# Kernel tuning notes

Measured on AMD Instinct MI355X. Metric: run time of the kernel, lower is better.

The kernel has to match this reference:

```python
import jax, jax.numpy as jnp
import numpy as np

BATCH, SEQ, D_IN, D_HID, D_OUT = 256, 512, 128, 128, 128


def setup_inputs() -> dict:
    key = jax.random.key(0)
    ks = jax.random.split(key, 10)
    def xavier(k, shape):
        std = (2.0 / (shape[0] + shape[1])) ** 0.5
        return jax.random.normal(k, shape, dtype=jnp.float32) * std
    return {
        "x": jax.random.normal(ks[0], (BATCH, SEQ, D_IN), dtype=jnp.float32),
        "x2i": xavier(ks[1], (D_IN, D_HID)),
        "x2f": xavier(ks[2], (D_IN, D_HID)),
        "x2g": xavier(ks[3], (D_IN, D_HID)),
        "x2o": xavier(ks[4], (D_IN, D_HID)),
        "h2i": xavier(ks[5], (D_HID, D_HID)),
        "h2f": xavier(ks[6], (D_HID, D_HID)),
        "h2g": xavier(ks[7], (D_HID, D_HID)),
        "h2o": xavier(ks[8], (D_HID, D_HID)),
        "w_out": xavier(ks[9], (D_HID, D_OUT)),
    }


def reference(x, x2i, x2f, x2g, x2o, h2i, h2f, h2g, h2o, w_out):
    batch = x.shape[0]
    hid = h2i.shape[0]
    # Precompute input projections for all timesteps (same math, hoisted out
    # of the recurrence): [B, S, 4H] -> time-major [S, B, 4H]
    wx = jnp.concatenate([x2i, x2f, x2g, x2o], axis=1)       # [D_IN, 4H]
    wh = jnp.concatenate([h2i, h2f, h2g, h2o], axis=1)       # [H, 4H]
    xg = jnp.einsum("bsi,ik->sbk", x, wx)                    # [S, B, 4H]

    def step(carry, xg_t):
        c, h = carry
        gates = xg_t + h @ wh                                # [B, 4H]
        i = jax.nn.sigmoid(gates[:, 0 * hid:1 * hid])
        f = jax.nn.sigmoid(gates[:, 1 * hid:2 * hid])
        g = jnp.tanh(gates[:, 2 * hid:3 * hid])
        o = jax.nn.sigmoid(gates[:, 3 * hid:4 * hid])
        c = f * c + i * g
        h = o * jnp.tanh(c)
        return (c, h), None

    c0 = jnp.zeros((batch, hid), dtype=x.dtype)
    h0 = jnp.zeros((batch, hid), dtype=x.dtype)
    (c_T, h_T), _ = jax.lax.scan(step, (c0, h0), xg)
    return h_T @ w_out
```

## Files before the change

### kernel.cpp

```cpp
#include <hip/hip_runtime.h>

typedef unsigned int u32;
typedef __fp16 half2_t __attribute__((ext_vector_type(2)));
typedef __fp16 half8_t __attribute__((ext_vector_type(8)));
typedef float  f32x4   __attribute__((ext_vector_type(4)));

#define DIN 128
#define DH  128
#define SEQL 512
#define NBATCH 256
#define NC  512
#define TC  64
#define NCHUNK (SEQL/TC)

#define LDS_HOFF 65536
#define LDS_TOTAL (65536 + 512)

__device__ __forceinline__ u32 pk2(float a, float b) {
  half2_t h = __builtin_amdgcn_cvt_pkrtz(a, b);
  return __builtin_bit_cast(u32, h);
}

__device__ __forceinline__ float dot2(u32 a, u32 b, float c) {
#if defined(__has_builtin) && __has_builtin(__builtin_amdgcn_fdot2)
  return __builtin_amdgcn_fdot2(__builtin_bit_cast(half2_t, a),
                                __builtin_bit_cast(half2_t, b), c, false);
#else
  half2_t ha = __builtin_bit_cast(half2_t, a);
  half2_t hb = __builtin_bit_cast(half2_t, b);
  return c + (float)ha[0]*(float)hb[0] + (float)ha[1]*(float)hb[1];
#endif
}

#if defined(__has_builtin) && __has_builtin(__builtin_amdgcn_update_dpp)
__device__ __forceinline__ float qp_xor1(float v) {
  return __builtin_bit_cast(float,
      __builtin_amdgcn_update_dpp(0, __builtin_bit_cast(int, v), 0xB1, 0xF, 0xF, true));
}
__device__ __forceinline__ float qp_xor2(float v) {
  return __builtin_bit_cast(float,
      __builtin_amdgcn_update_dpp(0, __builtin_bit_cast(int, v), 0x4E, 0xF, 0xF, true));
}
#else
__device__ __forceinline__ float qp_xor1(float v) { return __shfl_xor(v, 1, 64); }
__device__ __forceinline__ float qp_xor2(float v) { return __shfl_xor(v, 2, 64); }
#endif

__device__ __forceinline__ float fexp2(float x) {
#if defined(__has_builtin) && __has_builtin(__builtin_amdgcn_exp2f)
  return __builtin_amdgcn_exp2f(x);
#else
  return __builtin_exp2f(x);
#endif
}

#define DOT16(S, W, H0, H1, H2, H3) \
  S = dot2((W)[0].x, (H0).x, S); S = dot2((W)[0].y, (H0).y, S); \
  S = dot2((W)[0].z, (H0).z, S); S = dot2((W)[0].w, (H0).w, S); \
  S = dot2((W)[1].x, (H1).x, S); S = dot2((W)[1].y, (H1).y, S); \
  S = dot2((W)[1].z, (H1).z, S); S = dot2((W)[1].w, (H1).w, S); \
  S = dot2((W)[2].x, (H2).x, S); S = dot2((W)[2].y, (H2).y, S); \
  S = dot2((W)[2].z, (H2).z, S); S = dot2((W)[2].w, (H2).w, S); \
  S = dot2((W)[3].x, (H3).x, S); S = dot2((W)[3].y, (H3).y, S); \
  S = dot2((W)[3].z, (H3).z, S); S = dot2((W)[3].w, (H3).w, S);

__global__ void pack_w(const float* __restrict__ x2i, const float* __restrict__ x2f,
                       const float* __restrict__ x2g, const float* __restrict__ x2o,
                       const float* __restrict__ h2i, const float* __restrict__ h2f,
                       const float* __restrict__ h2g, const float* __restrict__ h2o,
                       u32* __restrict__ wxT, u32* __restrict__ whT) {
  int idx = blockIdx.x * blockDim.x + threadIdx.x;
  if (idx >= NC * 64) return;
  int j = idx >> 6, kk = idx & 63;
  int g = j >> 7, jjj = j & 127;
  const float* wx = (g == 0) ? x2i : (g == 1) ? x2f : (g == 2) ? x2g : x2o;
  const float* wh = (g == 0) ? h2i : (g == 1) ? h2f : (g == 2) ? h2g : h2o;
  wxT[idx] = pk2(wx[(2*kk)*DH + jjj], wx[(2*kk+1)*DH + jjj]);
  whT[idx] = pk2(wh[(2*kk)*DH + jjj], wh[(2*kk+1)*DH + jjj]);
}

__global__ __launch_bounds__(512, 2) void lstm_fused(
    const float* __restrict__ x, const u32* __restrict__ wxT,
    const u32* __restrict__ whT, const float* __restrict__ w_out,
    float* __restrict__ out) {
  extern __shared__ char lds[];
  char* xgT  = lds;
  u32*  hbuf = (u32*)(lds + LDS_HOFF);

  const int tid = threadIdx.x;
  const int b   = blockIdx.x;
  const int l   = tid & 63, wv = tid >> 6;
  const int kq  = l & 3, jj = l >> 2;
  const int colB = kq * DH + wv * 16 + jj;
  const int j    = wv * 16 + jj;
  const int kg = l >> 4, r15 = l & 15;

  uint4 wq[4][4];
#pragma unroll
  for (int q = 0; q < 4; ++q) {
    const uint4* wp = (const uint4*)(whT + (q * DH + j) * 64 + kq * 16);
#pragma unroll
    for (int mm = 0; mm < 4; ++mm) wq[q][mm] = wp[mm];
  }

  if (tid < 128) hbuf[tid] = 0u;
  float c = 0.f;
  u32 rdoff = LDS_HOFF + kq * 64;
  u32 wroff = LDS_HOFF + 256 + j * 2;
  const bool isG = (kq == 2);
  const float mexp = isG ? -2.885390082f : -1.442695041f;
  const bool k1 = (kq & 1) != 0, k2 = (kq & 2) != 0;

  const float* xb = x + (size_t)b * SEQL * DIN;
  __syncthreads();

  for (int ch = 0; ch < NCHUNK; ++ch) {
#pragma unroll 1
    for (int tt = 0; tt < 4; ++tt) {
      uint4 afr[4];
#pragma unroll
      for (int ko = 0; ko < 4; ++ko) {
        const float4* xp = (const float4*)(xb + (size_t)(ch*TC + tt*16 + r15)*DIN + ko*32 + kg*8);
        float4 v0 = xp[0], v1 = xp[1];
        afr[ko].x = pk2(v0.x, v0.y); afr[ko].y = pk2(v0.z, v0.w);
        afr[ko].z = pk2(v1.x, v1.y); afr[ko].w = pk2(v1.z, v1.w);
      }
#pragma unroll
      for (int nt = 0; nt < 4; ++nt) {
        int n = wv * 64 + nt * 16 + r15;
        f32x4 acc = {0.f, 0.f, 0.f, 0.f};
#pragma unroll
        for (int ko = 0; ko < 4; ++ko) {
          uint4 bf = *(const uint4*)(wxT + n*64 + ko*16 + kg*4);
          acc = __builtin_amdgcn_mfma_f32_16x16x32_f16(
              __builtin_bit_cast(half8_t, afr[ko]),
              __builtin_bit_cast(half8_t, bf), acc, 0, 0, 0);
        }
        int t0 = tt*16 + kg*4;
        u32 off = (u32)(n*128 + ((t0*2) ^ ((n & 7) << 4)));
        uint2 pw; pw.x = pk2(acc[0], acc[1]); pw.y = pk2(acc[2], acc[3]);
        *(uint2*)(xgT + off) = pw;
      }
    }
    __syncthreads();

#pragma unroll 1
    for (int m = 0; m < 8; ++m) {
      uint4 xgv = *(const uint4*)(xgT + colB*128 + ((m*16) ^ ((colB & 7) << 4)));
      half8_t xgh = __builtin_bit_cast(half8_t, xgv);
#pragma unroll
      for (int s8 = 0; s8 < 8; ++s8) {
        uint4 h0 = *(const uint4*)(lds + rdoff);
        uint4 h1 = *(const uint4*)(lds + rdoff + 16);
        uint4 h2 = *(const uint4*)(lds + rdoff + 32);
        uint4 h3 = *(const uint4*)(lds + rdoff + 48);
        float s0 = 0.f, s1 = 0.f, s2 = 0.f, s3 = 0.f;
        DOT16(s0, wq[0], h0, h1, h2, h3)
        DOT16(s1, wq[1], h0, h1, h2, h3)
        DOT16(s2, wq[2], h0, h1, h2, h3)
        DOT16(s3, wq[3], h0, h1, h2, h3)
        s0 += qp_xor1(s0); s0 += qp_xor2(s0);
        s1 += qp_xor1(s1); s1 += qp_xor2(s1);
        s2 += qp_xor1(s2); s2 += qp_xor2(s2);
        s3 += qp_xor1(s3); s3 += qp_xor2(s3);
        float t01 = k1 ? s1 : s0;
        float t23 = k1 ? s3 : s2;
        float tk  = (k2 ? t23 : t01) + (float)xgh[s8];
        float e   = fexp2(tk * mexp);
        float y   = __builtin_amdgcn_rcpf(1.f + e);
        float val = isG ? __builtin_fmaf(2.f, y, -1.f) : y;
        float vb = qp_xor1(val);
        float x0 = k1 ? vb : val;
        float x1 = k1 ? val : vb;
        float y2 = qp_xor2(x0);
        float y3 = qp_xor2(x1);
        float gi = k2 ? y2 : x0;
        float gf = k2 ? y3 : x1;
        float gg = k2 ? x0 : y2;
        float go = k2 ? x1 : y3;
        c = __builtin_fmaf(gf, c, gi * gg);
        float e2 = fexp2(c * -2.885390082f);
        float th = __builtin_fmaf(2.f, __builtin_amdgcn_rcpf(1.f + e2), -1.f);
        float hval = go * th;
        if (kq == 0) *(__fp16*)(lds + wroff) = (__fp16)hval;
        rdoff ^= 256; wroff ^= 256;
        __syncthreads();
      }
    }
  }

  if (tid < DH) {
    int n = tid;
    const u32* hf = (const u32*)(lds + (rdoff & ~(u32)255));
    float acc = 0.f;
#pragma unroll 8
    for (int kk = 0; kk < 64; ++kk) {
      half2_t h2v = __builtin_bit_cast(half2_t, hf[kk]);
      acc = __builtin_fmaf((float)h2v[0], w_out[(2*kk)*DH + n],
            __builtin_fmaf((float)h2v[1], w_out[(2*kk+1)*DH + n], acc));
    }
    out[b * DH + n] = acc;
  }
}

extern "C" void kernel_launch(void* const* d_in, const int* in_sizes, int n_in,
                              void* d_out, int out_size, void* d_ws, size_t ws_size,
                              hipStream_t stream) {
  const float* x    = (const float*)d_in[0];
  const float* x2i  = (const float*)d_in[1];
  const float* x2f  = (const float*)d_in[2];
  const float* x2g  = (const float*)d_in[3];
  const float* x2o  = (const float*)d_in[4];
  const float* h2i  = (const float*)d_in[5];
  const float* h2f  = (const float*)d_in[6];
  const float* h2g  = (const float*)d_in[7];
  const float* h2o  = (const float*)d_in[8];
  const float* wout = (const float*)d_in[9];

  u32* wxT = (u32*)d_ws;
  u32* whT = wxT + NC * 64;

  (void)hipFuncSetAttribute((const void*)lstm_fused,
                            hipFuncAttributeMaxDynamicSharedMemorySize, LDS_TOTAL);

  pack_w<<<64, 512, 0, stream>>>(x2i, x2f, x2g, x2o, h2i, h2f, h2g, h2o, wxT, whT);
  lstm_fused<<<NBATCH, 512, LDS_TOTAL, stream>>>(x, wxT, whT, wout, (float*)d_out);
}
```

Baseline: 319.7 us.

## Compute recurrent gate matvec with MFMA instead of packed dot2 reductions

Replaces the per-step h·Wh product, previously done with fdot2 chains and DPP cross-lane reductions, with 16 MFMA 16x16x32 f16 instructions per wave. Each wave holds its Wh slice as B fragments, and h is broadcast as the A operand. Each lane then computes all four gates directly, so the cross-lane gate shuffles go away. In exchange, each MFMA's output is only one-sixteenth useful, and every lane evaluates five transcendental functions per step instead of two.

```diff
diff --git a/kernel.cpp b/kernel.cpp
--- a/kernel.cpp
+++ b/kernel.cpp
@@ -21,31 +21,6 @@
   return __builtin_bit_cast(u32, h);
 }
 
-__device__ __forceinline__ float dot2(u32 a, u32 b, float c) {
-#if defined(__has_builtin) && __has_builtin(__builtin_amdgcn_fdot2)
-  return __builtin_amdgcn_fdot2(__builtin_bit_cast(half2_t, a),
-                                __builtin_bit_cast(half2_t, b), c, false);
-#else
-  half2_t ha = __builtin_bit_cast(half2_t, a);
-  half2_t hb = __builtin_bit_cast(half2_t, b);
-  return c + (float)ha[0]*(float)hb[0] + (float)ha[1]*(float)hb[1];
-#endif
-}
-
-#if defined(__has_builtin) && __has_builtin(__builtin_amdgcn_update_dpp)
-__device__ __forceinline__ float qp_xor1(float v) {
-  return __builtin_bit_cast(float,
-      __builtin_amdgcn_update_dpp(0, __builtin_bit_cast(int, v), 0xB1, 0xF, 0xF, true));
-}
-__device__ __forceinline__ float qp_xor2(float v) {
-  return __builtin_bit_cast(float,
-      __builtin_amdgcn_update_dpp(0, __builtin_bit_cast(int, v), 0x4E, 0xF, 0xF, true));
-}
-#else
-__device__ __forceinline__ float qp_xor1(float v) { return __shfl_xor(v, 1, 64); }
-__device__ __forceinline__ float qp_xor2(float v) { return __shfl_xor(v, 2, 64); }
-#endif
-
 __device__ __forceinline__ float fexp2(float x) {
 #if defined(__has_builtin) && __has_builtin(__builtin_amdgcn_exp2f)
   return __builtin_amdgcn_exp2f(x);
@@ -54,15 +29,8 @@
 #endif
 }
 
-#define DOT16(S, W, H0, H1, H2, H3) \
-  S = dot2((W)[0].x, (H0).x, S); S = dot2((W)[0].y, (H0).y, S); \
-  S = dot2((W)[0].z, (H0).z, S); S = dot2((W)[0].w, (H0).w, S); \
-  S = dot2((W)[1].x, (H1).x, S); S = dot2((W)[1].y, (H1).y, S); \
-  S = dot2((W)[1].z, (H1).z, S); S = dot2((W)[1].w, (H1).w, S); \
-  S = dot2((W)[2].x, (H2).x, S); S = dot2((W)[2].y, (H2).y, S); \
-  S = dot2((W)[2].z, (H2).z, S); S = dot2((W)[2].w, (H2).w, S); \
-  S = dot2((W)[3].x, (H3).x, S); S = dot2((W)[3].y, (H3).y, S); \
-  S = dot2((W)[3].z, (H3).z, S); S = dot2((W)[3].w, (H3).w, S);
+#define MF(A, B, C) __builtin_amdgcn_mfma_f32_16x16x32_f16( \
+    __builtin_bit_cast(half8_t, A), __builtin_bit_cast(half8_t, B), C, 0, 0, 0)
 
 __global__ void pack_w(const float* __restrict__ x2i, const float* __restrict__ x2f,
                        const float* __restrict__ x2g, const float* __restrict__ x2o,
@@ -79,38 +47,31 @@
   whT[idx] = pk2(wh[(2*kk)*DH + jjj], wh[(2*kk+1)*DH + jjj]);
 }
 
-__global__ __launch_bounds__(512, 2) void lstm_fused(
+__global__ __launch_bounds__(512, 2)
+void lstm_fused(
     const float* __restrict__ x, const u32* __restrict__ wxT,
     const u32* __restrict__ whT, const float* __restrict__ w_out,
     float* __restrict__ out) {
   extern __shared__ char lds[];
-  char* xgT  = lds;
-  u32*  hbuf = (u32*)(lds + LDS_HOFF);
+  char* xgT = lds;
 
   const int tid = threadIdx.x;
   const int b   = blockIdx.x;
   const int l   = tid & 63, wv = tid >> 6;
-  const int kq  = l & 3, jj = l >> 2;
-  const int colB = kq * DH + wv * 16 + jj;
-  const int j    = wv * 16 + jj;
-  const int kg = l >> 4, r15 = l & 15;
+  const int kg  = l >> 4, r15 = l & 15;
 
-  uint4 wq[4][4];
+  uint4 bw[4][4];
 #pragma unroll
-  for (int q = 0; q < 4; ++q) {
-    const uint4* wp = (const uint4*)(whT + (q * DH + j) * 64 + kq * 16);
+  for (int g = 0; g < 4; ++g) {
+    const uint4* wp = (const uint4*)(whT + (g * DH + wv * 16 + r15) * 64);
 #pragma unroll
-    for (int mm = 0; mm < 4; ++mm) wq[q][mm] = wp[mm];
+    for (int kt = 0; kt < 4; ++kt) bw[g][kt] = wp[kt * 4 + kg];
   }
 
-  if (tid < 128) hbuf[tid] = 0u;
+  if (tid < 128) ((u32*)(lds + LDS_HOFF))[tid] = 0u;
   float c = 0.f;
-  u32 rdoff = LDS_HOFF + kq * 64;
-  u32 wroff = LDS_HOFF + 256 + j * 2;
-  const bool isG = (kq == 2);
-  const float mexp = isG ? -2.885390082f : -1.442695041f;
-  const bool k1 = (kq & 1) != 0, k2 = (kq & 2) != 0;
-
+  u32 rdh = LDS_HOFF;
+  u32 wrh = LDS_HOFF + 256;
   const float* xb = x + (size_t)b * SEQL * DIN;
   __syncthreads();
 
@@ -132,9 +93,7 @@
 #pragma unroll
         for (int ko = 0; ko < 4; ++ko) {
           uint4 bf = *(const uint4*)(wxT + n*64 + ko*16 + kg*4);
-          acc = __builtin_amdgcn_mfma_f32_16x16x32_f16(
-              __builtin_bit_cast(half8_t, afr[ko]),
-              __builtin_bit_cast(half8_t, bf), acc, 0, 0, 0);
+          acc = MF(afr[ko], bf, acc);
         }
         int t0 = tt*16 + kg*4;
         u32 off = (u32)(n*128 + ((t0*2) ^ ((n & 7) << 4)));
@@ -146,44 +105,44 @@
 
 #pragma unroll 1
     for (int m = 0; m < 8; ++m) {
-      uint4 xgv = *(const uint4*)(xgT + colB*128 + ((m*16) ^ ((colB & 7) << 4)));
-      half8_t xgh = __builtin_bit_cast(half8_t, xgv);
+      half8_t xh[4];
+#pragma unroll
+      for (int g = 0; g < 4; ++g) {
+        int cg = g * DH + wv * 16 + r15;
+        xh[g] = __builtin_bit_cast(half8_t,
+            *(const uint4*)(xgT + cg*128 + ((m*16) ^ ((cg & 7) << 4))));
+      }
 #pragma unroll
       for (int s8 = 0; s8 < 8; ++s8) {
-        uint4 h0 = *(const uint4*)(lds + rdoff);
-        uint4 h1 = *(const uint4*)(lds + rdoff + 16);
-        uint4 h2 = *(const uint4*)(lds + rdoff + 32);
-        uint4 h3 = *(const uint4*)(lds + rdoff + 48);
-        float s0 = 0.f, s1 = 0.f, s2 = 0.f, s3 = 0.f;
-        DOT16(s0, wq[0], h0, h1, h2, h3)
-        DOT16(s1, wq[1], h0, h1, h2, h3)
-        DOT16(s2, wq[2], h0, h1, h2, h3)
-        DOT16(s3, wq[3], h0, h1, h2, h3)
-        s0 += qp_xor1(s0); s0 += qp_xor2(s0);
-        s1 += qp_xor1(s1); s1 += qp_xor2(s1);
-        s2 += qp_xor1(s2); s2 += qp_xor2(s2);
-        s3 += qp_xor1(s3); s3 += qp_xor2(s3);
-        float t01 = k1 ? s1 : s0;
-        float t23 = k1 ? s3 : s2;
-        float tk  = (k2 ? t23 : t01) + (float)xgh[s8];
-        float e   = fexp2(tk * mexp);
-        float y   = __builtin_amdgcn_rcpf(1.f + e);
-        float val = isG ? __builtin_fmaf(2.f, y, -1.f) : y;
-        float vb = qp_xor1(val);
-        float x0 = k1 ? vb : val;
-        float x1 = k1 ? val : vb;
-        float y2 = qp_xor2(x0);
-        float y3 = qp_xor2(x1);
-        float gi = k2 ? y2 : x0;
-        float gf = k2 ? y3 : x1;
-        float gg = k2 ? x0 : y2;
-        float go = k2 ? x1 : y3;
-        c = __builtin_fmaf(gf, c, gi * gg);
-        float e2 = fexp2(c * -2.885390082f);
-        float th = __builtin_fmaf(2.f, __builtin_amdgcn_rcpf(1.f + e2), -1.f);
-        float hval = go * th;
-        if (kq == 0) *(__fp16*)(lds + wroff) = (__fp16)hval;
-        rdoff ^= 256; wroff ^= 256;
+        uint4 a0 = *(const uint4*)(lds + rdh +   0 + kg*16);
+        uint4 a1 = *(const uint4*)(lds + rdh +  64 + kg*16);
+        uint4 a2 = *(const uint4*)(lds + rdh + 128 + kg*16);
+        uint4 a3 = *(const uint4*)(lds + rdh + 192 + kg*16);
+        f32x4 z = {0.f, 0.f, 0.f, 0.f};
+        f32x4 aci = z, acf = z, acg = z, aco = z;
+        aci = MF(a0, bw[0][0], aci); acf = MF(a0, bw[1][0], acf);
+        acg = MF(a0, bw[2][0], acg); aco = MF(a0, bw[3][0], aco);
+        aci = MF(a1, bw[0][1], aci); acf = MF(a1, bw[1][1], acf);
+        acg = MF(a1, bw[2][1], acg); aco = MF(a1, bw[3][1], aco);
+        aci = MF(a2, bw[0][2], aci); acf = MF(a2, bw[1][2], acf);
+        acg = MF(a2, bw[2][2], acg); aco = MF(a2, bw[3][2], aco);
+        aci = MF(a3, bw[0][3], aci); acf = MF(a3, bw[1][3], acf);
+        acg = MF(a3, bw[2][3], acg); aco = MF(a3, bw[3][3], aco);
+        float gi = aci[0] + (float)xh[0][s8];
+        float gf = acf[0] + (float)xh[1][s8];
+        float gg = acg[0] + (float)xh[2][s8];
+        float go = aco[0] + (float)xh[3][s8];
+        float si = __builtin_amdgcn_rcpf(1.f + fexp2(gi * -1.442695041f));
+        float sf = __builtin_amdgcn_rcpf(1.f + fexp2(gf * -1.442695041f));
+        float sg = __builtin_fmaf(2.f,
+                     __builtin_amdgcn_rcpf(1.f + fexp2(gg * -2.885390082f)), -1.f);
+        float so = __builtin_amdgcn_rcpf(1.f + fexp2(go * -1.442695041f));
+        c = __builtin_fmaf(sf, c, si * sg);
+        float th = __builtin_fmaf(2.f,
+                     __builtin_amdgcn_rcpf(1.f + fexp2(c * -2.885390082f)), -1.f);
+        float hval = so * th;
+        if (l < 16) *(__fp16*)(lds + wrh + (wv * 16 + l) * 2) = (__fp16)hval;
+        u32 tswap = rdh; rdh = wrh; wrh = tswap;
         __syncthreads();
       }
     }
@@ -191,7 +150,7 @@
 
   if (tid < DH) {
     int n = tid;
-    const u32* hf = (const u32*)(lds + (rdoff & ~(u32)255));
+    const u32* hf = (const u32*)(lds + rdh);
     float acc = 0.f;
 #pragma unroll 8
     for (int kk = 0; kk < 64; ++kk) {
```

Result: faster. 288.7 us (-9.7%).
